# Optimization experiments

Measured on AMD Instinct MI355X. Metric: run time of the kernel, lower is better.

## Reference

```python
import jax, jax.numpy as jnp
import numpy as np

N, C, H, E = 10000, 128, 256, 320000
CUTOFF = 5.0
EPS = 1e-5


def _ln(x, g, b):
    mu = jnp.mean(x, axis=-1, keepdims=True)
    var = jnp.var(x, axis=-1, keepdims=True)
    return (x - mu) * jax.lax.rsqrt(var + EPS) * g + b


def setup_inputs() -> dict:
    key = jax.random.key(0)
    ks = jax.random.split(key, 24)

    def w(k, shape, fan_in):
        return (jax.random.normal(k, shape, dtype=jnp.float32) / np.sqrt(fan_in)).astype(jnp.float32)

    inp = {}
    inp["x"] = jax.random.normal(ks[0], (N, 3), dtype=jnp.float32)
    inp["h"] = jax.random.normal(ks[1], (N, C), dtype=jnp.float32)
    inp["edge_index"] = jax.random.randint(ks[2], (2, E), 0, N, dtype=jnp.int32)
    # edge_mlp: Linear(2C+1 -> H), SiLU, Linear(H -> H), SiLU
    inp["We1"] = w(ks[3], (2 * C + 1, H), 2 * C + 1); inp["be1"] = jnp.zeros((H,), jnp.float32)
    inp["We2"] = w(ks[4], (H, H), H);                inp["be2"] = jnp.zeros((H,), jnp.float32)
    # node_mlp: Linear(C+H -> H), SiLU, Linear(H -> C)
    inp["Wn1"] = w(ks[5], (C + H, H), C + H);        inp["bn1"] = jnp.zeros((H,), jnp.float32)
    inp["Wn2"] = w(ks[6], (H, C), H);                inp["bn2"] = jnp.zeros((C,), jnp.float32)
    # residual mlp: Linear(C -> H), SiLU, Dropout(eval), Linear(H -> C)
    inp["Wm1"] = w(ks[7], (C, H), C);                inp["bm1"] = jnp.zeros((H,), jnp.float32)
    inp["Wm2"] = w(ks[8], (H, C), H);                inp["bm2"] = jnp.zeros((C,), jnp.float32)
    # layernorms
    inp["g1"] = jnp.ones((C,), jnp.float32); inp["beta1"] = jnp.zeros((C,), jnp.float32)
    inp["g2"] = jnp.ones((C,), jnp.float32); inp["beta2"] = jnp.zeros((C,), jnp.float32)
    return inp


def reference(x, h, edge_index, We1, be1, We2, be2, Wn1, bn1, Wn2, bn2,
              Wm1, bm1, Wm2, bm2, g1, beta1, g2, beta2):
    row, col = edge_index[0], edge_index[1]

    h_res = h
    hn = _ln(h, g1, beta1)                              # [N, C]

    # ---- EGNN layer ----
    rel = x[row] - x[col]                               # [E, 3]
    dist = jnp.linalg.norm(rel, axis=-1, keepdims=True) # [E, 1]
    edge_in = jnp.concatenate([hn[row], hn[col], dist], axis=-1)  # [E, 2C+1]
    m = jax.nn.silu(edge_in @ We1 + be1)
    m = jax.nn.silu(m @ We2 + be2)                      # [E, H]

    d = dist[:, 0]
    Ccut = 0.5 * (jnp.cos(d * jnp.pi / CUTOFF) + 1.0)
    Ccut = Ccut * (d <= CUTOFF) * (d >= 0.0)
    m = m * Ccut[:, None]

    # mean-aggregate messages at target nodes (edge_index[1])
    sums = jax.ops.segment_sum(m, col, num_segments=N)          # [N, H]
    cnt = jax.ops.segment_sum(jnp.ones((m.shape[0],), m.dtype), col, num_segments=N)
    m_aggr = sums / jnp.maximum(cnt, 1.0)[:, None]

    hd = jax.nn.silu(jnp.concatenate([hn, m_aggr], axis=-1) @ Wn1 + bn1) @ Wn2 + bn2
    h_egnn = hn + hd

    h1 = h_res + h_egnn

    # ---- norm2 + MLP residual (dropout = identity in eval) ----
    h2 = _ln(h1, g2, beta2)
    h2 = jax.nn.silu(h2 @ Wm1 + bm1) @ Wm2 + bm2
    return h1 + h2
```

## Files before the change

### kernel.cpp

```cpp
#include <hip/hip_runtime.h>

#define NN 10000
#define CC 128
#define HH 256
#define EE 320000
#define ETILE 96
#define EBLOCKS 3334

typedef __bf16 bf16_t;
typedef __bf16 bf16x8 __attribute__((ext_vector_type(8)));
typedef __bf16 bf16x4 __attribute__((ext_vector_type(4)));
typedef float f32x4 __attribute__((ext_vector_type(4)));

__device__ __forceinline__ float silu_f(float v) {
#if __has_builtin(__builtin_amdgcn_rcpf)
  return v * __builtin_amdgcn_rcpf(1.0f + __expf(-v));
#else
  return v / (1.0f + __expf(-v));
#endif
}

template<int RE, int KD, int SA, int NT>
__device__ __forceinline__ void gemm_lg(const bf16_t* sAa, const bf16_t* __restrict__ BT,
                                        int nwavebase, int lr, int quad, f32x4 acc[RE][NT]) {
  for (int kk = 0; kk < KD; kk += 32) {
    bf16x8 a[RE]; bf16x8 b[NT];
#pragma unroll
    for (int re = 0; re < RE; re++)
      a[re] = *(const bf16x8*)(sAa + (re * 16 + lr) * SA + kk + quad * 8);
#pragma unroll
    for (int ce = 0; ce < NT; ce++)
      b[ce] = *(const bf16x8*)(BT + (size_t)(nwavebase + ce * 16 + lr) * KD + kk + quad * 8);
#pragma unroll
    for (int re = 0; re < RE; re++)
#pragma unroll
      for (int ce = 0; ce < NT; ce++)
        acc[re][ce] = __builtin_amdgcn_mfma_f32_16x16x32_bf16(a[re], b[ce], acc[re][ce], 0, 0, 0);
  }
}

__global__ __launch_bounds__(256) void prep_weights(
    const float* __restrict__ We1, const float* __restrict__ We2,
    const float* __restrict__ Wn1, const float* __restrict__ Wn2,
    const float* __restrict__ Wm1, const float* __restrict__ Wm2,
    bf16_t* __restrict__ We1T, bf16_t* __restrict__ We2T,
    bf16_t* __restrict__ Wn1T, bf16_t* __restrict__ Wn2T,
    bf16_t* __restrict__ Wm1T, bf16_t* __restrict__ Wm2T) {
  int i = blockIdx.x * 256 + threadIdx.x;
  const float* src; bf16_t* dst; int K, Nc, idx;
  if      (i < 65536)  { src = We1; dst = We1T; K = 256; Nc = 256; idx = i; }
  else if (i < 131072) { src = We2; dst = We2T; K = 256; Nc = 256; idx = i - 65536; }
  else if (i < 229376) { src = Wn1; dst = Wn1T; K = 384; Nc = 256; idx = i - 131072; }
  else if (i < 262144) { src = Wn2; dst = Wn2T; K = 256; Nc = 128; idx = i - 229376; }
  else if (i < 294912) { src = Wm1; dst = Wm1T; K = 128; Nc = 256; idx = i - 262144; }
  else                 { src = Wm2; dst = Wm2T; K = 256; Nc = 128; idx = i - 294912; }
  int n = idx / K, k = idx - n * K;
  dst[idx] = (bf16_t)src[(size_t)k * Nc + n];
}

__global__ __launch_bounds__(256, 3) void node_pre_kernel(
    const float* __restrict__ h, const float* __restrict__ g1,
    const float* __restrict__ bt1,
    const bf16_t* __restrict__ We1T, const float* __restrict__ be1,
    bf16_t* __restrict__ hn16, bf16_t* __restrict__ PQ) {
  __shared__ __align__(16) float sHf[64 * 132];
  __shared__ __align__(16) bf16_t sHn[64 * 136];
  int tid = threadIdx.x;
  int lane = tid & 63, wave = tid >> 6;
  int lr = lane & 15, quad = lane >> 4;
  int n0 = blockIdx.x * 64;

#pragma unroll
  for (int i = 0; i < 8; i++) {
    int o = tid + i * 256;
    int node = o >> 5, q = o & 31;
    f32x4 v = {0.f, 0.f, 0.f, 0.f};
    if (n0 + node < NN) v = *(const f32x4*)(h + (size_t)(n0 + node) * CC + q * 4);
    *(f32x4*)(sHf + node * 132 + q * 4) = v;
  }
  __syncthreads();

  {
    int node = tid >> 2, c0 = (tid & 3) * 32;
    f32x4 u[8];
    float s = 0.f, sq = 0.f;
#pragma unroll
    for (int j = 0; j < 8; j++) {
      u[j] = *(const f32x4*)(sHf + node * 132 + c0 + j * 4);
#pragma unroll
      for (int r = 0; r < 4; r++) { s += u[j][r]; sq += u[j][r] * u[j][r]; }
    }
    s += __shfl_xor(s, 1); sq += __shfl_xor(sq, 1);
    s += __shfl_xor(s, 2); sq += __shfl_xor(sq, 2);
    float mu = s * (1.0f / CC);
    float var = sq * (1.0f / CC) - mu * mu;
    float rs = rsqrtf(var + 1e-5f);
    bool live = (n0 + node) < NN;
#pragma unroll
    for (int j2 = 0; j2 < 4; j2++) {
      f32x4 gg0 = *(const f32x4*)(g1 + c0 + j2 * 8);
      f32x4 gg1 = *(const f32x4*)(g1 + c0 + j2 * 8 + 4);
      f32x4 bb0 = *(const f32x4*)(bt1 + c0 + j2 * 8);
      f32x4 bb1 = *(const f32x4*)(bt1 + c0 + j2 * 8 + 4);
      bf16x8 ov;
#pragma unroll
      for (int r = 0; r < 4; r++) {
        ov[r] = (bf16_t)((u[j2 * 2][r] - mu) * rs * gg0[r] + bb0[r]);
        ov[r + 4] = (bf16_t)((u[j2 * 2 + 1][r] - mu) * rs * gg1[r] + bb1[r]);
      }
      *(bf16x8*)(sHn + node * 136 + c0 + j2 * 8) = ov;
      if (live) *(bf16x8*)(hn16 + (size_t)(n0 + node) * CC + c0 + j2 * 8) = ov;
    }
  }
  __syncthreads();

  f32x4 zf = {0.f, 0.f, 0.f, 0.f};
#pragma unroll
  for (int p = 0; p < 2; p++) {
    f32x4 acc[4][4];
#pragma unroll
    for (int i = 0; i < 4; i++)
#pragma unroll
      for (int j = 0; j < 4; j++) acc[i][j] = zf;
    for (int kk = 0; kk < 128; kk += 32) {
      bf16x8 a[4]; bf16x8 b[4];
#pragma unroll
      for (int re = 0; re < 4; re++)
        a[re] = *(const bf16x8*)(We1T + (size_t)(wave * 64 + re * 16 + lr) * 256 + p * 128 + kk + quad * 8);
#pragma unroll
      for (int ce = 0; ce < 4; ce++)
        b[ce] = *(const bf16x8*)(sHn + (ce * 16 + lr) * 136 + kk + quad * 8);
#pragma unroll
      for (int re = 0; re < 4; re++)
#pragma unroll
        for (int ce = 0; ce < 4; ce++)
          acc[re][ce] = __builtin_amdgcn_mfma_f32_16x16x32_bf16(a[re], b[ce], acc[re][ce], 0, 0, 0);
    }
#pragma unroll
    for (int re = 0; re < 4; re++) {
      int cbase = wave * 64 + re * 16 + quad * 4;
      f32x4 bb = zf;
      if (p == 0) bb = *(const f32x4*)(be1 + cbase);
#pragma unroll
      for (int ce = 0; ce < 4; ce++) {
        int node = ce * 16 + lr;
        if (n0 + node < NN) {
          bf16x4 o;
#pragma unroll
          for (int r = 0; r < 4; r++) o[r] = (bf16_t)(acc[re][ce][r] + bb[r]);
          *(bf16x4*)(PQ + (size_t)(n0 + node) * 512 + p * 256 + cbase) = o;
        }
      }
    }
  }
}

__global__ __launch_bounds__(256) void count_kernel(const int* __restrict__ ei, int* __restrict__ cnt) {
  int e = blockIdx.x * 256 + threadIdx.x;
  atomicAdd(&cnt[ei[EE + e]], 1);
}

__global__ __launch_bounds__(1024) void scan_kernel(const int* __restrict__ cnt, int* __restrict__ cursor) {
  __shared__ int wsum[16];
  int tid = threadIdx.x, wave = tid >> 6, lane = tid & 63;
  int base = 0;
  for (int start = 0; start < NN; start += 1024) {
    int i = start + tid;
    int v = (i < NN) ? cnt[i] : 0;
    int s = v;
#pragma unroll
    for (int off = 1; off < 64; off <<= 1) { int t = __shfl_up(s, off); if (lane >= off) s += t; }
    if (lane == 63) wsum[wave] = s;
    __syncthreads();
    if (tid < 16) {
      int ws = wsum[tid];
#pragma unroll
      for (int off = 1; off < 16; off <<= 1) { int t = __shfl_up(ws, off); if (tid >= off) ws += t; }
      wsum[tid] = ws;
    }
    __syncthreads();
    int wp = (wave > 0) ? wsum[wave - 1] : 0;
    if (i < NN) cursor[i] = base + wp + s - v;
    base += wsum[15];
    __syncthreads();
  }
}

__global__ __launch_bounds__(256) void scatter_kernel(const int* __restrict__ ei,
                                                      const float* __restrict__ x,
                                                      int* __restrict__ cursor,
                                                      uint4* __restrict__ edat) {
  int e = blockIdx.x * 256 + threadIdx.x;
  int r = ei[e], c = ei[EE + e];
  float dx = x[3 * r] - x[3 * c];
  float dy = x[3 * r + 1] - x[3 * c + 1];
  float dz = x[3 * r + 2] - x[3 * c + 2];
  float d = sqrtf(dx * dx + dy * dy + dz * dz);
  float cc = (d <= 5.0f) ? 0.5f * (cosf(d * 0.6283185307179586f) + 1.0f) : 0.0f;
  int pos = atomicAdd(&cursor[c], 1);
  uint4 v = {(unsigned)r, (unsigned)c, __float_as_uint(d), __float_as_uint(cc)};
  edat[pos] = v;
}

__global__ __launch_bounds__(256, 3) void edge_mlp_kernel(
    const uint4* __restrict__ edat, const bf16_t* __restrict__ PQ,
    const float* __restrict__ We1last,
    const bf16_t* __restrict__ We2T, const float* __restrict__ be2,
    float* __restrict__ sums) {
  __shared__ __align__(16) bf16_t sM1[ETILE * 264];
  __shared__ int sRow[ETILE], sCol[ETILE];
  __shared__ float sD[ETILE], sCc[ETILE];
  __shared__ unsigned long long sMask[2];
  int tid = threadIdx.x;
  int lane = tid & 63, wave = tid >> 6;
  int lr = lane & 15, quad = lane >> 4;
  int e0 = blockIdx.x * ETILE;

  if (tid < ETILE) {
    uint4 v = edat[e0 + tid];
    sRow[tid] = (int)v.x; sCol[tid] = (int)v.y;
    sD[tid] = __uint_as_float(v.z); sCc[tid] = __uint_as_float(v.w);
  }
  __syncthreads();

  if (tid < ETILE) {
    int fl = (tid > 0) && (sCol[tid] != sCol[tid - 1]);
    unsigned long long m = __ballot(fl);
    if ((tid & 63) == 0) sMask[wave] = m;
  }

#pragma unroll
  for (int i = 0; i < ETILE * 32 / 256; i++) {
    int o = tid + i * 256;
    int e = o >> 5, q = o & 31;
    int k0 = q * 8;
    int row = sRow[e], col = sCol[e];
    float d = sD[e];
    bf16x8 pv = *(const bf16x8*)(PQ + (size_t)row * 512 + k0);
    bf16x8 qv = *(const bf16x8*)(PQ + (size_t)col * 512 + 256 + k0);
    f32x4 wl0 = *(const f32x4*)(We1last + k0);
    f32x4 wl1 = *(const f32x4*)(We1last + k0 + 4);
    bf16x8 m;
#pragma unroll
    for (int j = 0; j < 4; j++) {
      m[j] = (bf16_t)silu_f((float)pv[j] + (float)qv[j] + d * wl0[j]);
      m[j + 4] = (bf16_t)silu_f((float)pv[j + 4] + (float)qv[j + 4] + d * wl1[j]);
    }
    *(bf16x8*)(sM1 + e * 264 + k0) = m;
  }
  __syncthreads();

  f32x4 zf = {0.f, 0.f, 0.f, 0.f};
  f32x4 acc[6][4];
#pragma unroll
  for (int i = 0; i < 6; i++)
#pragma unroll
    for (int j = 0; j < 4; j++) acc[i][j] = zf;
  gemm_lg<6, 256, 264, 4>(sM1, We2T, wave * 64, lr, quad, acc);

  float be2v[4];
#pragma unroll
  for (int ce = 0; ce < 4; ce++) be2v[ce] = be2[wave * 64 + ce * 16 + lr];
#pragma unroll
  for (int re = 0; re < 6; re++) {
    f32x4 cc = *(const f32x4*)(sCc + re * 16 + quad * 4);
#pragma unroll
    for (int ce = 0; ce < 4; ce++)
#pragma unroll
      for (int r = 0; r < 4; r++)
        acc[re][ce][r] = silu_f(acc[re][ce][r] + be2v[ce]) * cc[r];
  }

  {
    unsigned long long w0 = sMask[0];
    unsigned long long w1 = sMask[1];
    int lo = 0;
    while (lo < ETILE) {
      int hi;
      unsigned long long t = (lo < 63) ? (w0 & (~0ull << (lo + 1))) : 0ull;
      if (t) {
        hi = __ffsll((long long)t) - 1;
      } else {
        unsigned long long mk = (lo + 1 > 64) ? (~0ull << (lo + 1 - 64)) : ~0ull;
        unsigned long long t1 = w1 & mk;
        hi = t1 ? 64 + __ffsll((long long)t1) - 1 : ETILE;
      }
      f32x4 tv = zf;
#pragma unroll
      for (int re = 0; re < 6; re++) {
        int eb = re * 16 + quad * 4;
#pragma unroll
        for (int r = 0; r < 4; r++) {
          int e = eb + r;
          bool in = (e >= lo) && (e < hi);
#pragma unroll
          for (int ce = 0; ce < 4; ce++)
            tv[ce] += in ? acc[re][ce][r] : 0.0f;
        }
      }
#pragma unroll
      for (int ce = 0; ce < 4; ce++) {
        tv[ce] += __shfl_xor(tv[ce], 16);
        tv[ce] += __shfl_xor(tv[ce], 32);
      }
      if (quad == 0) {
        int colv = sCol[lo];
#pragma unroll
        for (int ce = 0; ce < 4; ce++)
          atomicAdd(&sums[(size_t)colv * HH + wave * 64 + ce * 16 + lr], tv[ce]);
      }
      lo = hi;
    }
  }
}

__global__ __launch_bounds__(256) void node_fused_kernel(
    const float* __restrict__ h, const bf16_t* __restrict__ hn16,
    const float* __restrict__ sums, const int* __restrict__ cnt,
    const bf16_t* __restrict__ Wn1T, const float* __restrict__ bn1,
    const bf16_t* __restrict__ Wn2T, const float* __restrict__ bn2,
    const float* __restrict__ g2, const float* __restrict__ bt2,
    const bf16_t* __restrict__ Wm1T, const float* __restrict__ bm1,
    const bf16_t* __restrict__ Wm2T, const float* __restrict__ bm2,
    float* __restrict__ out) {
  __shared__ __align__(16) bf16_t sA1[16 * 392];
  __shared__ __align__(16) bf16_t sM[16 * 264];
  __shared__ __align__(16) float sH1[16 * 132];
  __shared__ __align__(16) bf16_t sLn[16 * 136];
  __shared__ float sRc[16];
  int tid = threadIdx.x;
  int lane = tid & 63, wave = tid >> 6;
  int lr = lane & 15, quad = lane >> 4;
  int n0 = blockIdx.x * 16;

  if (tid < 16) sRc[tid] = 1.0f / fmaxf((float)cnt[n0 + tid], 1.0f);
  __syncthreads();

#pragma unroll
  for (int i = 0; i < 3; i++) {
    int o = tid + i * 256;
    int e = o / 48, q = o - e * 48;
    int node = n0 + e;
    if (q < 16) {
      *(uint4*)(sA1 + e * 392 + q * 8) = *(const uint4*)(hn16 + (size_t)node * CC + q * 8);
    } else {
      float rc = sRc[e];
      const float* sp = sums + (size_t)node * HH + (q - 16) * 8;
      bf16x8 bv;
#pragma unroll
      for (int k2 = 0; k2 < 8; k2++) bv[k2] = (bf16_t)(sp[k2] * rc);
      *(bf16x8*)(sA1 + e * 392 + (q - 16) * 8 + 128) = bv;
    }
  }
  __syncthreads();

  f32x4 zf = {0.f, 0.f, 0.f, 0.f};
  {
    f32x4 acc[1][4];
#pragma unroll
    for (int j = 0; j < 4; j++) acc[0][j] = zf;
    gemm_lg<1, 384, 392, 4>(sA1, Wn1T, wave * 64, lr, quad, acc);
#pragma unroll
    for (int ce = 0; ce < 4; ce++) {
      int n = wave * 64 + ce * 16 + lr;
      float b1 = bn1[n];
#pragma unroll
      for (int r = 0; r < 4; r++)
        sM[(quad * 4 + r) * 264 + n] = (bf16_t)silu_f(acc[0][ce][r] + b1);
    }
  }
  __syncthreads();

  {
    f32x4 acc[1][2];
    acc[0][0] = zf; acc[0][1] = zf;
    gemm_lg<1, 256, 264, 2>(sM, Wn2T, wave * 32, lr, quad, acc);
#pragma unroll
    for (int ce = 0; ce < 2; ce++) {
      int n = wave * 32 + ce * 16 + lr;
      float b2 = bn2[n];
#pragma unroll
      for (int r = 0; r < 4; r++) {
        int node = quad * 4 + r;
        size_t idx = (size_t)(n0 + node) * CC + n;
        float hn_v = (float)sA1[node * 392 + n];
        sH1[node * 132 + n] = h[idx] + hn_v + acc[0][ce][r] + b2;
      }
    }
  }
  __syncthreads();

  {
    int node = tid >> 4, c0 = (tid & 15) * 8;
    f32x4 u0 = *(const f32x4*)(sH1 + node * 132 + c0);
    f32x4 u1 = *(const f32x4*)(sH1 + node * 132 + c0 + 4);
    float s = 0.f, sq = 0.f;
#pragma unroll
    for (int j = 0; j < 4; j++) { s += u0[j] + u1[j]; sq += u0[j] * u0[j] + u1[j] * u1[j]; }
#pragma unroll
    for (int o = 8; o > 0; o >>= 1) { s += __shfl_xor(s, o); sq += __shfl_xor(sq, o); }
    float mu = s * (1.0f / CC);
    float var = sq * (1.0f / CC) - mu * mu;
    float rs = rsqrtf(var + 1e-5f);
    f32x4 gg0 = *(const f32x4*)(g2 + c0), gg1 = *(const f32x4*)(g2 + c0 + 4);
    f32x4 bb0 = *(const f32x4*)(bt2 + c0), bb1 = *(const f32x4*)(bt2 + c0 + 4);
    bf16x8 ov;
#pragma unroll
    for (int j = 0; j < 4; j++) {
      ov[j] = (bf16_t)((u0[j] - mu) * rs * gg0[j] + bb0[j]);
      ov[j + 4] = (bf16_t)((u1[j] - mu) * rs * gg1[j] + bb1[j]);
    }
    *(bf16x8*)(sLn + node * 136 + c0) = ov;
  }
  __syncthreads();

  {
    f32x4 acc[1][4];
#pragma unroll
    for (int j = 0; j < 4; j++) acc[0][j] = zf;
    gemm_lg<1, 128, 136, 4>(sLn, Wm1T, wave * 64, lr, quad, acc);
#pragma unroll
    for (int ce = 0; ce < 4; ce++) {
      int n = wave * 64 + ce * 16 + lr;
      float b1 = bm1[n];
#pragma unroll
      for (int r = 0; r < 4; r++)
        sM[(quad * 4 + r) * 264 + n] = (bf16_t)silu_f(acc[0][ce][r] + b1);
    }
  }
  __syncthreads();

  {
    f32x4 acc[1][2];
    acc[0][0] = zf; acc[0][1] = zf;
    gemm_lg<1, 256, 264, 2>(sM, Wm2T, wave * 32, lr, quad, acc);
#pragma unroll
    for (int ce = 0; ce < 2; ce++) {
      int n = wave * 32 + ce * 16 + lr;
      float b2 = bm2[n];
#pragma unroll
      for (int r = 0; r < 4; r++) {
        int node = quad * 4 + r;
        size_t idx = (size_t)(n0 + node) * CC + n;
        out[idx] = sH1[node * 132 + n] + acc[0][ce][r] + b2;
      }
    }
  }
}

extern "C" void kernel_launch(void* const* d_in, const int* in_sizes, int n_in,
                              void* d_out, int out_size, void* d_ws, size_t ws_size,
                              hipStream_t stream) {
  const float* x    = (const float*)d_in[0];
  const float* h    = (const float*)d_in[1];
  const int*   ei   = (const int*)d_in[2];
  const float* We1  = (const float*)d_in[3];
  const float* be1  = (const float*)d_in[4];
  const float* We2  = (const float*)d_in[5];
  const float* be2  = (const float*)d_in[6];
  const float* Wn1  = (const float*)d_in[7];
  const float* bn1  = (const float*)d_in[8];
  const float* Wn2  = (const float*)d_in[9];
  const float* bn2  = (const float*)d_in[10];
  const float* Wm1  = (const float*)d_in[11];
  const float* bm1  = (const float*)d_in[12];
  const float* Wm2  = (const float*)d_in[13];
  const float* bm2  = (const float*)d_in[14];
  const float* g1   = (const float*)d_in[15];
  const float* bt1  = (const float*)d_in[16];
  const float* g2   = (const float*)d_in[17];
  const float* bt2  = (const float*)d_in[18];
  float* out = (float*)d_out;

  char* wp = (char*)d_ws;
  size_t off = 0;
  auto alloc = [&](size_t bytes) -> void* {
    void* p = wp + off;
    off = (off + bytes + 255) & ~(size_t)255;
    return p;
  };

  bf16_t* hn16   = (bf16_t*)alloc((size_t)NN * CC * 2);
  bf16_t* PQ     = (bf16_t*)alloc((size_t)NN * 512 * 2);
  float*  sums   = (float*)alloc((size_t)NN * HH * 4);
  int*    cnt    = (int*)alloc((size_t)NN * 4);
  int*    cursor = (int*)alloc((size_t)NN * 4);
  uint4*  edat   = (uint4*)alloc((size_t)(EBLOCKS * ETILE) * 16);
  bf16_t* We1T   = (bf16_t*)alloc(256 * 256 * 2);
  bf16_t* We2T   = (bf16_t*)alloc(256 * 256 * 2);
  bf16_t* Wn1T   = (bf16_t*)alloc(256 * 384 * 2);
  bf16_t* Wn2T   = (bf16_t*)alloc(128 * 256 * 2);
  bf16_t* Wm1T   = (bf16_t*)alloc(256 * 128 * 2);
  bf16_t* Wm2T   = (bf16_t*)alloc(128 * 256 * 2);

  hipMemsetAsync(sums, 0, (size_t)NN * HH * 4, stream);
  hipMemsetAsync(cnt, 0, (size_t)NN * 4, stream);
  hipMemsetAsync(edat + EE, 0, (size_t)(EBLOCKS * ETILE - EE) * 16, stream);

  prep_weights<<<1280, 256, 0, stream>>>(We1, We2, Wn1, Wn2, Wm1, Wm2,
                                         We1T, We2T, Wn1T, Wn2T, Wm1T, Wm2T);

  node_pre_kernel<<<(NN + 63) / 64, 256, 0, stream>>>(h, g1, bt1, We1T, be1, hn16, PQ);

  count_kernel<<<EE / 256, 256, 0, stream>>>(ei, cnt);
  scan_kernel<<<1, 1024, 0, stream>>>(cnt, cursor);
  scatter_kernel<<<EE / 256, 256, 0, stream>>>(ei, x, cursor, edat);

  edge_mlp_kernel<<<EBLOCKS, 256, 0, stream>>>(edat, PQ, We1 + 256 * 256,
                                               We2T, be2, sums);

  node_fused_kernel<<<NN / 16, 256, 0, stream>>>(h, hn16, sums, cnt,
                                                 Wn1T, bn1, Wn2T, bn2,
                                                 g2, bt2, Wm1T, bm1, Wm2T, bm2, out);
}
```

Before: 311.7 us.

## Retile edge and node kernels, fold memsets into weight prep kernel

Shrinks the edge MLP tile from 96 to 64 edges (one mask word, 4 blocks per CU occupancy hint) and grows the node fused kernel from 16 to 64 nodes per block so each weight load feeds four MFMA row tiles. It also replaces the separate memset calls with zeroing inside the weight-prep kernel, cutting launch count. The larger node tile uses about 135KB of shared memory, which limits it to one block per CU, and the smaller edge tile means more segments cut at tile edges and more atomics.

```diff
diff --git a/kernel.cpp b/kernel.cpp
--- a/kernel.cpp
+++ b/kernel.cpp
@@ -4,8 +4,8 @@
 #define CC 128
 #define HH 256
 #define EE 320000
-#define ETILE 96
-#define EBLOCKS 3334
+#define ETILE 64
+#define EBLOCKS 5000
 
 typedef __bf16 bf16_t;
 typedef __bf16 bf16x8 __attribute__((ext_vector_type(8)));
@@ -39,23 +39,32 @@
   }
 }
 
-__global__ __launch_bounds__(256) void prep_weights(
+__global__ __launch_bounds__(256) void prep_kernel(
     const float* __restrict__ We1, const float* __restrict__ We2,
     const float* __restrict__ Wn1, const float* __restrict__ Wn2,
     const float* __restrict__ Wm1, const float* __restrict__ Wm2,
     bf16_t* __restrict__ We1T, bf16_t* __restrict__ We2T,
     bf16_t* __restrict__ Wn1T, bf16_t* __restrict__ Wn2T,
-    bf16_t* __restrict__ Wm1T, bf16_t* __restrict__ Wm2T) {
+    bf16_t* __restrict__ Wm1T, bf16_t* __restrict__ Wm2T,
+    float* __restrict__ sums, int* __restrict__ cnt) {
   int i = blockIdx.x * 256 + threadIdx.x;
-  const float* src; bf16_t* dst; int K, Nc, idx;
-  if      (i < 65536)  { src = We1; dst = We1T; K = 256; Nc = 256; idx = i; }
-  else if (i < 131072) { src = We2; dst = We2T; K = 256; Nc = 256; idx = i - 65536; }
-  else if (i < 229376) { src = Wn1; dst = Wn1T; K = 384; Nc = 256; idx = i - 131072; }
-  else if (i < 262144) { src = Wn2; dst = Wn2T; K = 256; Nc = 128; idx = i - 229376; }
-  else if (i < 294912) { src = Wm1; dst = Wm1T; K = 128; Nc = 256; idx = i - 262144; }
-  else                 { src = Wm2; dst = Wm2T; K = 256; Nc = 128; idx = i - 294912; }
-  int n = idx / K, k = idx - n * K;
-  dst[idx] = (bf16_t)src[(size_t)k * Nc + n];
+  if (i < 327680) {
+    const float* src; bf16_t* dst; int K, Nc, idx;
+    if      (i < 65536)  { src = We1; dst = We1T; K = 256; Nc = 256; idx = i; }
+    else if (i < 131072) { src = We2; dst = We2T; K = 256; Nc = 256; idx = i - 65536; }
+    else if (i < 229376) { src = Wn1; dst = Wn1T; K = 384; Nc = 256; idx = i - 131072; }
+    else if (i < 262144) { src = Wn2; dst = Wn2T; K = 256; Nc = 128; idx = i - 229376; }
+    else if (i < 294912) { src = Wm1; dst = Wm1T; K = 128; Nc = 256; idx = i - 262144; }
+    else                 { src = Wm2; dst = Wm2T; K = 256; Nc = 128; idx = i - 294912; }
+    int n = idx / K, k = idx - n * K;
+    dst[idx] = (bf16_t)src[(size_t)k * Nc + n];
+  } else if (i < 327680 + 640000) {
+    f32x4 z = {0.f, 0.f, 0.f, 0.f};
+    ((f32x4*)sums)[i - 327680] = z;
+  } else if (i < 327680 + 640000 + 2500) {
+    int4 z = {0, 0, 0, 0};
+    ((int4*)cnt)[i - 967680] = z;
+  }
 }
 
 __global__ __launch_bounds__(256, 3) void node_pre_kernel(
@@ -202,7 +211,7 @@
   edat[pos] = v;
 }
 
-__global__ __launch_bounds__(256, 3) void edge_mlp_kernel(
+__global__ __launch_bounds__(256, 4) void edge_mlp_kernel(
     const uint4* __restrict__ edat, const bf16_t* __restrict__ PQ,
     const float* __restrict__ We1last,
     const bf16_t* __restrict__ We2T, const float* __restrict__ be2,
@@ -210,7 +219,7 @@
   __shared__ __align__(16) bf16_t sM1[ETILE * 264];
   __shared__ int sRow[ETILE], sCol[ETILE];
   __shared__ float sD[ETILE], sCc[ETILE];
-  __shared__ unsigned long long sMask[2];
+  __shared__ unsigned long long sMask;
   int tid = threadIdx.x;
   int lane = tid & 63, wave = tid >> 6;
   int lr = lane & 15, quad = lane >> 4;
@@ -223,14 +232,14 @@
   }
   __syncthreads();
 
-  if (tid < ETILE) {
+  if (tid < 64) {
     int fl = (tid > 0) && (sCol[tid] != sCol[tid - 1]);
     unsigned long long m = __ballot(fl);
-    if ((tid & 63) == 0) sMask[wave] = m;
-  }
-
-#pragma unroll
-  for (int i = 0; i < ETILE * 32 / 256; i++) {
+    if (tid == 0) sMask = m;
+  }
+
+#pragma unroll
+  for (int i = 0; i < 8; i++) {
     int o = tid + i * 256;
     int e = o >> 5, q = o & 31;
     int k0 = q * 8;
@@ -251,18 +260,18 @@
   __syncthreads();
 
   f32x4 zf = {0.f, 0.f, 0.f, 0.f};
-  f32x4 acc[6][4];
-#pragma unroll
-  for (int i = 0; i < 6; i++)
+  f32x4 acc[4][4];
+#pragma unroll
+  for (int i = 0; i < 4; i++)
 #pragma unroll
     for (int j = 0; j < 4; j++) acc[i][j] = zf;
-  gemm_lg<6, 256, 264, 4>(sM1, We2T, wave * 64, lr, quad, acc);
+  gemm_lg<4, 256, 264, 4>(sM1, We2T, wave * 64, lr, quad, acc);
 
   float be2v[4];
 #pragma unroll
   for (int ce = 0; ce < 4; ce++) be2v[ce] = be2[wave * 64 + ce * 16 + lr];
 #pragma unroll
-  for (int re = 0; re < 6; re++) {
+  for (int re = 0; re < 4; re++) {
     f32x4 cc = *(const f32x4*)(sCc + re * 16 + quad * 4);
 #pragma unroll
     for (int ce = 0; ce < 4; ce++)
@@ -272,22 +281,14 @@
   }
 
   {
-    unsigned long long w0 = sMask[0];
-    unsigned long long w1 = sMask[1];
+    unsigned long long w0 = sMask;
     int lo = 0;
     while (lo < ETILE) {
-      int hi;
       unsigned long long t = (lo < 63) ? (w0 & (~0ull << (lo + 1))) : 0ull;
-      if (t) {
-        hi = __ffsll((long long)t) - 1;
-      } else {
-        unsigned long long mk = (lo + 1 > 64) ? (~0ull << (lo + 1 - 64)) : ~0ull;
-        unsigned long long t1 = w1 & mk;
-        hi = t1 ? 64 + __ffsll((long long)t1) - 1 : ETILE;
-      }
+      int hi = t ? (__ffsll((long long)t) - 1) : ETILE;
       f32x4 tv = zf;
 #pragma unroll
-      for (int re = 0; re < 6; re++) {
+      for (int re = 0; re < 4; re++) {
         int eb = re * 16 + quad * 4;
 #pragma unroll
         for (int r = 0; r < 4; r++) {
@@ -314,7 +315,7 @@
   }
 }
 
-__global__ __launch_bounds__(256) void node_fused_kernel(
+__global__ __launch_bounds__(256, 1) void node_fused_kernel(
     const float* __restrict__ h, const bf16_t* __restrict__ hn16,
     const float* __restrict__ sums, const int* __restrict__ cnt,
     const bf16_t* __restrict__ Wn1T, const float* __restrict__ bn1,
@@ -323,127 +324,171 @@
     const bf16_t* __restrict__ Wm1T, const float* __restrict__ bm1,
     const bf16_t* __restrict__ Wm2T, const float* __restrict__ bm2,
     float* __restrict__ out) {
-  __shared__ __align__(16) bf16_t sA1[16 * 392];
-  __shared__ __align__(16) bf16_t sM[16 * 264];
-  __shared__ __align__(16) float sH1[16 * 132];
-  __shared__ __align__(16) bf16_t sLn[16 * 136];
-  __shared__ float sRc[16];
+  __shared__ __align__(16) char smem[135168];
+  bf16_t* sA1 = (bf16_t*)smem;
+  bf16_t* sM1b = (bf16_t*)(smem + 50176);
+  float*  sH1 = (float*)(smem + 50176);
+  bf16_t* sLn = (bf16_t*)(smem + 83968);
+  bf16_t* sH2 = (bf16_t*)(smem + 101376);
+  __shared__ float sRc[64];
   int tid = threadIdx.x;
   int lane = tid & 63, wave = tid >> 6;
   int lr = lane & 15, quad = lane >> 4;
-  int n0 = blockIdx.x * 16;
-
-  if (tid < 16) sRc[tid] = 1.0f / fmaxf((float)cnt[n0 + tid], 1.0f);
-  __syncthreads();
-
-#pragma unroll
-  for (int i = 0; i < 3; i++) {
+  int n0 = blockIdx.x * 64;
+
+  if (tid < 64) {
+    int node = n0 + tid;
+    sRc[tid] = (node < NN) ? 1.0f / fmaxf((float)cnt[node], 1.0f) : 0.0f;
+  }
+  __syncthreads();
+
+#pragma unroll
+  for (int i = 0; i < 12; i++) {
     int o = tid + i * 256;
     int e = o / 48, q = o - e * 48;
     int node = n0 + e;
     if (q < 16) {
-      *(uint4*)(sA1 + e * 392 + q * 8) = *(const uint4*)(hn16 + (size_t)node * CC + q * 8);
+      uint4 v = {0u, 0u, 0u, 0u};
+      if (node < NN) v = *(const uint4*)(hn16 + (size_t)node * CC + q * 8);
+      *(uint4*)(sA1 + e * 392 + q * 8) = v;
     } else {
-      float rc = sRc[e];
-      const float* sp = sums + (size_t)node * HH + (q - 16) * 8;
-      bf16x8 bv;
-#pragma unroll
-      for (int k2 = 0; k2 < 8; k2++) bv[k2] = (bf16_t)(sp[k2] * rc);
-      *(bf16x8*)(sA1 + e * 392 + (q - 16) * 8 + 128) = bv;
+      bf16x8 bv = {};
+      if (node < NN) {
+        float rc = sRc[e];
+        const float* sp = sums + (size_t)node * HH + (q - 16) * 8;
+#pragma unroll
+        for (int k2 = 0; k2 < 8; k2++) bv[k2] = (bf16_t)(sp[k2] * rc);
+      }
+      *(bf16x8*)(sA1 + e * 392 + 128 + (q - 16) * 8) = bv;
     }
   }
   __syncthreads();
 
   f32x4 zf = {0.f, 0.f, 0.f, 0.f};
   {
-    f32x4 acc[1][4];
-#pragma unroll
-    for (int j = 0; j < 4; j++) acc[0][j] = zf;
-    gemm_lg<1, 384, 392, 4>(sA1, Wn1T, wave * 64, lr, quad, acc);
+    f32x4 acc[4][4];
+#pragma unroll
+    for (int i = 0; i < 4; i++)
+#pragma unroll
+      for (int j = 0; j < 4; j++) acc[i][j] = zf;
+    gemm_lg<4, 384, 392, 4>(sA1, Wn1T, wave * 64, lr, quad, acc);
+    __syncthreads();
 #pragma unroll
     for (int ce = 0; ce < 4; ce++) {
       int n = wave * 64 + ce * 16 + lr;
       float b1 = bn1[n];
 #pragma unroll
-      for (int r = 0; r < 4; r++)
-        sM[(quad * 4 + r) * 264 + n] = (bf16_t)silu_f(acc[0][ce][r] + b1);
-    }
-  }
-  __syncthreads();
-
-  {
-    f32x4 acc[1][2];
-    acc[0][0] = zf; acc[0][1] = zf;
-    gemm_lg<1, 256, 264, 2>(sM, Wn2T, wave * 32, lr, quad, acc);
+      for (int re = 0; re < 4; re++)
+#pragma unroll
+        for (int r = 0; r < 4; r++)
+          sM1b[(re * 16 + quad * 4 + r) * 264 + n] = (bf16_t)silu_f(acc[re][ce][r] + b1);
+    }
+  }
+  __syncthreads();
+
+  float h1v[4][2][4];
+  {
+    f32x4 acc[4][2];
+#pragma unroll
+    for (int i = 0; i < 4; i++) { acc[i][0] = zf; acc[i][1] = zf; }
+    gemm_lg<4, 256, 264, 2>(sM1b, Wn2T, wave * 32, lr, quad, acc);
 #pragma unroll
     for (int ce = 0; ce < 2; ce++) {
       int n = wave * 32 + ce * 16 + lr;
       float b2 = bn2[n];
 #pragma unroll
-      for (int r = 0; r < 4; r++) {
-        int node = quad * 4 + r;
-        size_t idx = (size_t)(n0 + node) * CC + n;
-        float hn_v = (float)sA1[node * 392 + n];
-        sH1[node * 132 + n] = h[idx] + hn_v + acc[0][ce][r] + b2;
-      }
-    }
-  }
-  __syncthreads();
-
-  {
-    int node = tid >> 4, c0 = (tid & 15) * 8;
-    f32x4 u0 = *(const f32x4*)(sH1 + node * 132 + c0);
-    f32x4 u1 = *(const f32x4*)(sH1 + node * 132 + c0 + 4);
+      for (int re = 0; re < 4; re++)
+#pragma unroll
+        for (int r = 0; r < 4; r++) {
+          int node = re * 16 + quad * 4 + r;
+          float hv = 0.f;
+          if (n0 + node < NN) hv = h[(size_t)(n0 + node) * CC + n];
+          h1v[re][ce][r] = hv + (float)sA1[node * 392 + n] + acc[re][ce][r] + b2;
+        }
+    }
+  }
+  __syncthreads();
+
+#pragma unroll
+  for (int ce = 0; ce < 2; ce++) {
+    int n = wave * 32 + ce * 16 + lr;
+#pragma unroll
+    for (int re = 0; re < 4; re++)
+#pragma unroll
+      for (int r = 0; r < 4; r++)
+        sH1[(re * 16 + quad * 4 + r) * 132 + n] = h1v[re][ce][r];
+  }
+  __syncthreads();
+
+  {
+    int node = tid >> 2, c0 = (tid & 3) * 32;
+    f32x4 u[8];
     float s = 0.f, sq = 0.f;
 #pragma unroll
-    for (int j = 0; j < 4; j++) { s += u0[j] + u1[j]; sq += u0[j] * u0[j] + u1[j] * u1[j]; }
-#pragma unroll
-    for (int o = 8; o > 0; o >>= 1) { s += __shfl_xor(s, o); sq += __shfl_xor(sq, o); }
+    for (int j = 0; j < 8; j++) {
+      u[j] = *(const f32x4*)(sH1 + node * 132 + c0 + j * 4);
+#pragma unroll
+      for (int r = 0; r < 4; r++) { s += u[j][r]; sq += u[j][r] * u[j][r]; }
+    }
+    s += __shfl_xor(s, 1); sq += __shfl_xor(sq, 1);
+    s += __shfl_xor(s, 2); sq += __shfl_xor(sq, 2);
     float mu = s * (1.0f / CC);
     float var = sq * (1.0f / CC) - mu * mu;
     float rs = rsqrtf(var + 1e-5f);
-    f32x4 gg0 = *(const f32x4*)(g2 + c0), gg1 = *(const f32x4*)(g2 + c0 + 4);
-    f32x4 bb0 = *(const f32x4*)(bt2 + c0), bb1 = *(const f32x4*)(bt2 + c0 + 4);
-    bf16x8 ov;
-#pragma unroll
-    for (int j = 0; j < 4; j++) {
-      ov[j] = (bf16_t)((u0[j] - mu) * rs * gg0[j] + bb0[j]);
-      ov[j + 4] = (bf16_t)((u1[j] - mu) * rs * gg1[j] + bb1[j]);
-    }
-    *(bf16x8*)(sLn + node * 136 + c0) = ov;
-  }
-  __syncthreads();
-
-  {
-    f32x4 acc[1][4];
-#pragma unroll
-    for (int j = 0; j < 4; j++) acc[0][j] = zf;
-    gemm_lg<1, 128, 136, 4>(sLn, Wm1T, wave * 64, lr, quad, acc);
+#pragma unroll
+    for (int j2 = 0; j2 < 4; j2++) {
+      f32x4 gg0 = *(const f32x4*)(g2 + c0 + j2 * 8);
+      f32x4 gg1 = *(const f32x4*)(g2 + c0 + j2 * 8 + 4);
+      f32x4 bb0 = *(const f32x4*)(bt2 + c0 + j2 * 8);
+      f32x4 bb1 = *(const f32x4*)(bt2 + c0 + j2 * 8 + 4);
+      bf16x8 ov;
+#pragma unroll
+      for (int r = 0; r < 4; r++) {
+        ov[r] = (bf16_t)((u[j2 * 2][r] - mu) * rs * gg0[r] + bb0[r]);
+        ov[r + 4] = (bf16_t)((u[j2 * 2 + 1][r] - mu) * rs * gg1[r] + bb1[r]);
+      }
+      *(bf16x8*)(sLn + node * 136 + c0 + j2 * 8) = ov;
+    }
+  }
+  __syncthreads();
+
+  {
+    f32x4 acc[4][4];
+#pragma unroll
+    for (int i = 0; i < 4; i++)
+#pragma unroll
+      for (int j = 0; j < 4; j++) acc[i][j] = zf;
+    gemm_lg<4, 128, 136, 4>(sLn, Wm1T, wave * 64, lr, quad, acc);
 #pragma unroll
     for (int ce = 0; ce < 4; ce++) {
       int n = wave * 64 + ce * 16 + lr;
       float b1 = bm1[n];
 #pragma unroll
-      for (int r = 0; r < 4; r++)
-        sM[(quad * 4 + r) * 264 + n] = (bf16_t)silu_f(acc[0][ce][r] + b1);
-    }
-  }
-  __syncthreads();
-
-  {
-    f32x4 acc[1][2];
-    acc[0][0] = zf; acc[0][1] = zf;
-    gemm_lg<1, 256, 264, 2>(sM, Wm2T, wave * 32, lr, quad, acc);
+      for (int re = 0; re < 4; re++)
+#pragma unroll
+        for (int r = 0; r < 4; r++)
+          sH2[(re * 16 + quad * 4 + r) * 264 + n] = (bf16_t)silu_f(acc[re][ce][r] + b1);
+    }
+  }
+  __syncthreads();
+
+  {
+    f32x4 acc[4][2];
+#pragma unroll
+    for (int i = 0; i < 4; i++) { acc[i][0] = zf; acc[i][1] = zf; }
+    gemm_lg<4, 256, 264, 2>(sH2, Wm2T, wave * 32, lr, quad, acc);
 #pragma unroll
     for (int ce = 0; ce < 2; ce++) {
       int n = wave * 32 + ce * 16 + lr;
       float b2 = bm2[n];
 #pragma unroll
-      for (int r = 0; r < 4; r++) {
-        int node = quad * 4 + r;
-        size_t idx = (size_t)(n0 + node) * CC + n;
-        out[idx] = sH1[node * 132 + n] + acc[0][ce][r] + b2;
-      }
+      for (int re = 0; re < 4; re++)
+#pragma unroll
+        for (int r = 0; r < 4; r++) {
+          int node = re * 16 + quad * 4 + r;
+          if (n0 + node < NN)
+            out[(size_t)(n0 + node) * CC + n] = sH1[node * 132 + n] + acc[re][ce][r] + b2;
+        }
     }
   }
 }
@@ -485,7 +530,7 @@
   float*  sums   = (float*)alloc((size_t)NN * HH * 4);
   int*    cnt    = (int*)alloc((size_t)NN * 4);
   int*    cursor = (int*)alloc((size_t)NN * 4);
-  uint4*  edat   = (uint4*)alloc((size_t)(EBLOCKS * ETILE) * 16);
+  uint4*  edat   = (uint4*)alloc((size_t)EE * 16);
   bf16_t* We1T   = (bf16_t*)alloc(256 * 256 * 2);
   bf16_t* We2T   = (bf16_t*)alloc(256 * 256 * 2);
   bf16_t* Wn1T   = (bf16_t*)alloc(256 * 384 * 2);
@@ -493,12 +538,9 @@
   bf16_t* Wm1T   = (bf16_t*)alloc(256 * 128 * 2);
   bf16_t* Wm2T   = (bf16_t*)alloc(128 * 256 * 2);
 
-  hipMemsetAsync(sums, 0, (size_t)NN * HH * 4, stream);
-  hipMemsetAsync(cnt, 0, (size_t)NN * 4, stream);
-  hipMemsetAsync(edat + EE, 0, (size_t)(EBLOCKS * ETILE - EE) * 16, stream);
-
-  prep_weights<<<1280, 256, 0, stream>>>(We1, We2, Wn1, Wn2, Wm1, Wm2,
-                                         We1T, We2T, Wn1T, Wn2T, Wm1T, Wm2T);
+  prep_kernel<<<3790, 256, 0, stream>>>(We1, We2, Wn1, Wn2, Wm1, Wm2,
+                                        We1T, We2T, Wn1T, Wn2T, Wm1T, Wm2T,
+                                        sums, cnt);
 
   node_pre_kernel<<<(NN + 63) / 64, 256, 0, stream>>>(h, g1, bt1, We1T, be1, hn16, PQ);
 
@@ -509,7 +551,7 @@
   edge_mlp_kernel<<<EBLOCKS, 256, 0, stream>>>(edat, PQ, We1 + 256 * 256,
                                                We2T, be2, sums);
 
-  node_fused_kernel<<<NN / 16, 256, 0, stream>>>(h, hn16, sums, cnt,
-                                                 Wn1T, bn1, Wn2T, bn2,
-                                                 g2, bt2, Wm1T, bm1, Wm2T, bm2, out);
-}
+  node_fused_kernel<<<(NN + 63) / 64, 256, 0, stream>>>(h, hn16, sums, cnt,
+                                                        Wn1T, bn1, Wn2T, bn2,
+                                                        g2, bt2, Wm1T, bm1, Wm2T, bm2, out);
+}
```

After: 311.0 us. About the same (-0.2%).

## Fold memsets into prep kernel, retile node_pre, single-pass scan, faster segment reduce

Applied to the files above, without the earlier changes.

Replaces three hipMemsetAsync calls with zeroing work folded into the weight-prep kernel, which removes separate launches. The node_pre kernel is retiled to 16 nodes per block with direct global loads and a per-wave split of P/Q outputs. The scan becomes a single pass with 10 elements per thread, and the edge segment reduction skips or fully sums 16-row tiles instead of masking every element. Occupancy hints are also adjusted. Together these trade larger per-thread work and more blocks for fewer launches and less masking overhead.

```diff
diff --git a/kernel.cpp b/kernel.cpp
--- a/kernel.cpp
+++ b/kernel.cpp
@@ -39,119 +39,99 @@
   }
 }
 
-__global__ __launch_bounds__(256) void prep_weights(
+__global__ __launch_bounds__(256) void prep_kernel(
     const float* __restrict__ We1, const float* __restrict__ We2,
     const float* __restrict__ Wn1, const float* __restrict__ Wn2,
     const float* __restrict__ Wm1, const float* __restrict__ Wm2,
     bf16_t* __restrict__ We1T, bf16_t* __restrict__ We2T,
     bf16_t* __restrict__ Wn1T, bf16_t* __restrict__ Wn2T,
-    bf16_t* __restrict__ Wm1T, bf16_t* __restrict__ Wm2T) {
+    bf16_t* __restrict__ Wm1T, bf16_t* __restrict__ Wm2T,
+    float* __restrict__ sums, int* __restrict__ cnt, uint4* __restrict__ edat) {
   int i = blockIdx.x * 256 + threadIdx.x;
-  const float* src; bf16_t* dst; int K, Nc, idx;
-  if      (i < 65536)  { src = We1; dst = We1T; K = 256; Nc = 256; idx = i; }
-  else if (i < 131072) { src = We2; dst = We2T; K = 256; Nc = 256; idx = i - 65536; }
-  else if (i < 229376) { src = Wn1; dst = Wn1T; K = 384; Nc = 256; idx = i - 131072; }
-  else if (i < 262144) { src = Wn2; dst = Wn2T; K = 256; Nc = 128; idx = i - 229376; }
-  else if (i < 294912) { src = Wm1; dst = Wm1T; K = 128; Nc = 256; idx = i - 262144; }
-  else                 { src = Wm2; dst = Wm2T; K = 256; Nc = 128; idx = i - 294912; }
-  int n = idx / K, k = idx - n * K;
-  dst[idx] = (bf16_t)src[(size_t)k * Nc + n];
-}
-
-__global__ __launch_bounds__(256, 3) void node_pre_kernel(
+  if (i < 327680) {
+    const float* src; bf16_t* dst; int K, Nc, idx;
+    if      (i < 65536)  { src = We1; dst = We1T; K = 256; Nc = 256; idx = i; }
+    else if (i < 131072) { src = We2; dst = We2T; K = 256; Nc = 256; idx = i - 65536; }
+    else if (i < 229376) { src = Wn1; dst = Wn1T; K = 384; Nc = 256; idx = i - 131072; }
+    else if (i < 262144) { src = Wn2; dst = Wn2T; K = 256; Nc = 128; idx = i - 229376; }
+    else if (i < 294912) { src = Wm1; dst = Wm1T; K = 128; Nc = 256; idx = i - 262144; }
+    else                 { src = Wm2; dst = Wm2T; K = 256; Nc = 128; idx = i - 294912; }
+    int n = idx / K, k = idx - n * K;
+    dst[idx] = (bf16_t)src[(size_t)k * Nc + n];
+  } else if (i < 327680 + 640000) {
+    f32x4 z = {0.f, 0.f, 0.f, 0.f};
+    ((f32x4*)sums)[i - 327680] = z;
+  } else if (i < 327680 + 640000 + 2500) {
+    int4 z = {0, 0, 0, 0};
+    ((int4*)cnt)[i - 967680] = z;
+  } else if (i < 327680 + 640000 + 2500 + 64) {
+    uint4 z = {0u, 0u, 0u, 0u};
+    edat[EE + (i - 970180)] = z;
+  }
+}
+
+__global__ __launch_bounds__(256, 4) void node_pre_kernel(
     const float* __restrict__ h, const float* __restrict__ g1,
     const float* __restrict__ bt1,
     const bf16_t* __restrict__ We1T, const float* __restrict__ be1,
     bf16_t* __restrict__ hn16, bf16_t* __restrict__ PQ) {
-  __shared__ __align__(16) float sHf[64 * 132];
-  __shared__ __align__(16) bf16_t sHn[64 * 136];
+  __shared__ __align__(16) bf16_t sHn[16 * 136];
   int tid = threadIdx.x;
   int lane = tid & 63, wave = tid >> 6;
   int lr = lane & 15, quad = lane >> 4;
-  int n0 = blockIdx.x * 64;
-
-#pragma unroll
-  for (int i = 0; i < 8; i++) {
-    int o = tid + i * 256;
-    int node = o >> 5, q = o & 31;
-    f32x4 v = {0.f, 0.f, 0.f, 0.f};
-    if (n0 + node < NN) v = *(const f32x4*)(h + (size_t)(n0 + node) * CC + q * 4);
-    *(f32x4*)(sHf + node * 132 + q * 4) = v;
-  }
-  __syncthreads();
-
-  {
-    int node = tid >> 2, c0 = (tid & 3) * 32;
-    f32x4 u[8];
+  int n0 = blockIdx.x * 16;
+
+  {
+    int node = tid >> 4, c0 = (tid & 15) * 8;
+    size_t base = (size_t)(n0 + node) * CC;
+    f32x4 u0 = *(const f32x4*)(h + base + c0);
+    f32x4 u1 = *(const f32x4*)(h + base + c0 + 4);
     float s = 0.f, sq = 0.f;
 #pragma unroll
-    for (int j = 0; j < 8; j++) {
-      u[j] = *(const f32x4*)(sHf + node * 132 + c0 + j * 4);
-#pragma unroll
-      for (int r = 0; r < 4; r++) { s += u[j][r]; sq += u[j][r] * u[j][r]; }
-    }
-    s += __shfl_xor(s, 1); sq += __shfl_xor(sq, 1);
-    s += __shfl_xor(s, 2); sq += __shfl_xor(sq, 2);
+    for (int j = 0; j < 4; j++) { s += u0[j] + u1[j]; sq += u0[j] * u0[j] + u1[j] * u1[j]; }
+#pragma unroll
+    for (int o = 8; o > 0; o >>= 1) { s += __shfl_xor(s, o); sq += __shfl_xor(sq, o); }
     float mu = s * (1.0f / CC);
     float var = sq * (1.0f / CC) - mu * mu;
     float rs = rsqrtf(var + 1e-5f);
-    bool live = (n0 + node) < NN;
-#pragma unroll
-    for (int j2 = 0; j2 < 4; j2++) {
-      f32x4 gg0 = *(const f32x4*)(g1 + c0 + j2 * 8);
-      f32x4 gg1 = *(const f32x4*)(g1 + c0 + j2 * 8 + 4);
-      f32x4 bb0 = *(const f32x4*)(bt1 + c0 + j2 * 8);
-      f32x4 bb1 = *(const f32x4*)(bt1 + c0 + j2 * 8 + 4);
-      bf16x8 ov;
-#pragma unroll
-      for (int r = 0; r < 4; r++) {
-        ov[r] = (bf16_t)((u[j2 * 2][r] - mu) * rs * gg0[r] + bb0[r]);
-        ov[r + 4] = (bf16_t)((u[j2 * 2 + 1][r] - mu) * rs * gg1[r] + bb1[r]);
-      }
-      *(bf16x8*)(sHn + node * 136 + c0 + j2 * 8) = ov;
-      if (live) *(bf16x8*)(hn16 + (size_t)(n0 + node) * CC + c0 + j2 * 8) = ov;
-    }
-  }
-  __syncthreads();
-
+    f32x4 gg0 = *(const f32x4*)(g1 + c0), gg1 = *(const f32x4*)(g1 + c0 + 4);
+    f32x4 bb0 = *(const f32x4*)(bt1 + c0), bb1 = *(const f32x4*)(bt1 + c0 + 4);
+    bf16x8 ov;
+#pragma unroll
+    for (int j = 0; j < 4; j++) {
+      ov[j] = (bf16_t)((u0[j] - mu) * rs * gg0[j] + bb0[j]);
+      ov[j + 4] = (bf16_t)((u1[j] - mu) * rs * gg1[j] + bb1[j]);
+    }
+    *(bf16x8*)(sHn + node * 136 + c0) = ov;
+    *(bf16x8*)(hn16 + base + c0) = ov;
+  }
+  __syncthreads();
+
+  bool isQ = wave >= 2;
+  int rbase = (wave & 1) * 128;
+  int koff = isQ ? 128 : 0;
   f32x4 zf = {0.f, 0.f, 0.f, 0.f};
-#pragma unroll
-  for (int p = 0; p < 2; p++) {
-    f32x4 acc[4][4];
-#pragma unroll
-    for (int i = 0; i < 4; i++)
-#pragma unroll
-      for (int j = 0; j < 4; j++) acc[i][j] = zf;
-    for (int kk = 0; kk < 128; kk += 32) {
-      bf16x8 a[4]; bf16x8 b[4];
-#pragma unroll
-      for (int re = 0; re < 4; re++)
-        a[re] = *(const bf16x8*)(We1T + (size_t)(wave * 64 + re * 16 + lr) * 256 + p * 128 + kk + quad * 8);
-#pragma unroll
-      for (int ce = 0; ce < 4; ce++)
-        b[ce] = *(const bf16x8*)(sHn + (ce * 16 + lr) * 136 + kk + quad * 8);
-#pragma unroll
-      for (int re = 0; re < 4; re++)
-#pragma unroll
-        for (int ce = 0; ce < 4; ce++)
-          acc[re][ce] = __builtin_amdgcn_mfma_f32_16x16x32_bf16(a[re], b[ce], acc[re][ce], 0, 0, 0);
-    }
-#pragma unroll
-    for (int re = 0; re < 4; re++) {
-      int cbase = wave * 64 + re * 16 + quad * 4;
-      f32x4 bb = zf;
-      if (p == 0) bb = *(const f32x4*)(be1 + cbase);
-#pragma unroll
-      for (int ce = 0; ce < 4; ce++) {
-        int node = ce * 16 + lr;
-        if (n0 + node < NN) {
-          bf16x4 o;
-#pragma unroll
-          for (int r = 0; r < 4; r++) o[r] = (bf16_t)(acc[re][ce][r] + bb[r]);
-          *(bf16x4*)(PQ + (size_t)(n0 + node) * 512 + p * 256 + cbase) = o;
-        }
-      }
-    }
+  f32x4 acc[8];
+#pragma unroll
+  for (int i = 0; i < 8; i++) acc[i] = zf;
+  for (int kk = 0; kk < 128; kk += 32) {
+    bf16x8 b = *(const bf16x8*)(sHn + lr * 136 + kk + quad * 8);
+    bf16x8 a[8];
+#pragma unroll
+    for (int re = 0; re < 8; re++)
+      a[re] = *(const bf16x8*)(We1T + (size_t)(rbase + re * 16 + lr) * 256 + koff + kk + quad * 8);
+#pragma unroll
+    for (int re = 0; re < 8; re++)
+      acc[re] = __builtin_amdgcn_mfma_f32_16x16x32_bf16(a[re], b, acc[re], 0, 0, 0);
+  }
+#pragma unroll
+  for (int re = 0; re < 8; re++) {
+    int cb = rbase + re * 16 + quad * 4;
+    f32x4 bb = isQ ? zf : *(const f32x4*)(be1 + cb);
+    bf16x4 o;
+#pragma unroll
+    for (int r = 0; r < 4; r++) o[r] = (bf16_t)(acc[re][r] + bb[r]);
+    *(bf16x4*)(PQ + (size_t)(n0 + lr) * 512 + (isQ ? 256 : 0) + cb) = o;
   }
 }
 
@@ -163,26 +143,32 @@
 __global__ __launch_bounds__(1024) void scan_kernel(const int* __restrict__ cnt, int* __restrict__ cursor) {
   __shared__ int wsum[16];
   int tid = threadIdx.x, wave = tid >> 6, lane = tid & 63;
-  int base = 0;
-  for (int start = 0; start < NN; start += 1024) {
-    int i = start + tid;
-    int v = (i < NN) ? cnt[i] : 0;
-    int s = v;
-#pragma unroll
-    for (int off = 1; off < 64; off <<= 1) { int t = __shfl_up(s, off); if (lane >= off) s += t; }
-    if (lane == 63) wsum[wave] = s;
-    __syncthreads();
-    if (tid < 16) {
-      int ws = wsum[tid];
-#pragma unroll
-      for (int off = 1; off < 16; off <<= 1) { int t = __shfl_up(ws, off); if (tid >= off) ws += t; }
-      wsum[tid] = ws;
-    }
-    __syncthreads();
-    int wp = (wave > 0) ? wsum[wave - 1] : 0;
-    if (i < NN) cursor[i] = base + wp + s - v;
-    base += wsum[15];
-    __syncthreads();
+  int base = tid * 10;
+  int v[10]; int S = 0;
+#pragma unroll
+  for (int j = 0; j < 10; j++) {
+    int i = base + j;
+    v[j] = (i < NN) ? cnt[i] : 0;
+    S += v[j];
+  }
+  int s = S;
+#pragma unroll
+  for (int off = 1; off < 64; off <<= 1) { int t = __shfl_up(s, off); if (lane >= off) s += t; }
+  if (lane == 63) wsum[wave] = s;
+  __syncthreads();
+  if (tid < 16) {
+    int ws = wsum[tid];
+#pragma unroll
+    for (int off = 1; off < 16; off <<= 1) { int t = __shfl_up(ws, off); if (tid >= off) ws += t; }
+    wsum[tid] = ws;
+  }
+  __syncthreads();
+  int ex = ((wave > 0) ? wsum[wave - 1] : 0) + s - S;
+#pragma unroll
+  for (int j = 0; j < 10; j++) {
+    int i = base + j;
+    if (i < NN) cursor[i] = ex;
+    ex += v[j];
   }
 }
 
@@ -210,7 +196,8 @@
   __shared__ __align__(16) bf16_t sM1[ETILE * 264];
   __shared__ int sRow[ETILE], sCol[ETILE];
   __shared__ float sD[ETILE], sCc[ETILE];
-  __shared__ unsigned long long sMask[2];
+  __shared__ unsigned long long sMaskA;
+  __shared__ unsigned sMaskB;
   int tid = threadIdx.x;
   int lane = tid & 63, wave = tid >> 6;
   int lr = lane & 15, quad = lane >> 4;
@@ -226,7 +213,8 @@
   if (tid < ETILE) {
     int fl = (tid > 0) && (sCol[tid] != sCol[tid - 1]);
     unsigned long long m = __ballot(fl);
-    if ((tid & 63) == 0) sMask[wave] = m;
+    if (tid == 0) sMaskA = m;
+    if (tid == 64) sMaskB = (unsigned)m;
   }
 
 #pragma unroll
@@ -272,30 +260,40 @@
   }
 
   {
-    unsigned long long w0 = sMask[0];
-    unsigned long long w1 = sMask[1];
+    unsigned long long mA = sMaskA;
+    unsigned long long mB = (unsigned long long)sMaskB;
     int lo = 0;
     while (lo < ETILE) {
       int hi;
-      unsigned long long t = (lo < 63) ? (w0 & (~0ull << (lo + 1))) : 0ull;
-      if (t) {
-        hi = __ffsll((long long)t) - 1;
+      if (lo < 63) {
+        unsigned long long t = mA & (~0ull << (lo + 1));
+        hi = t ? (__ffsll((long long)t) - 1)
+               : (mB ? 64 + __ffsll((long long)mB) - 1 : ETILE);
       } else {
-        unsigned long long mk = (lo + 1 > 64) ? (~0ull << (lo + 1 - 64)) : ~0ull;
-        unsigned long long t1 = w1 & mk;
+        unsigned long long t1 = mB & (~0ull << (lo - 63));
         hi = t1 ? 64 + __ffsll((long long)t1) - 1 : ETILE;
       }
       f32x4 tv = zf;
 #pragma unroll
       for (int re = 0; re < 6; re++) {
-        int eb = re * 16 + quad * 4;
-#pragma unroll
-        for (int r = 0; r < 4; r++) {
-          int e = eb + r;
-          bool in = (e >= lo) && (e < hi);
-#pragma unroll
-          for (int ce = 0; ce < 4; ce++)
-            tv[ce] += in ? acc[re][ce][r] : 0.0f;
+        int t0 = re * 16, t1e = t0 + 16;
+        if (t1e <= lo || t0 >= hi) continue;
+        if (t0 >= lo && t1e <= hi) {
+#pragma unroll
+          for (int r = 0; r < 4; r++)
+#pragma unroll
+            for (int ce = 0; ce < 4; ce++)
+              tv[ce] += acc[re][ce][r];
+        } else {
+          int eb = t0 + quad * 4;
+#pragma unroll
+          for (int r = 0; r < 4; r++) {
+            int e = eb + r;
+            bool in = (e >= lo) && (e < hi);
+#pragma unroll
+            for (int ce = 0; ce < 4; ce++)
+              tv[ce] += in ? acc[re][ce][r] : 0.0f;
+          }
         }
       }
 #pragma unroll
@@ -314,7 +312,7 @@
   }
 }
 
-__global__ __launch_bounds__(256) void node_fused_kernel(
+__global__ __launch_bounds__(256, 3) void node_fused_kernel(
     const float* __restrict__ h, const bf16_t* __restrict__ hn16,
     const float* __restrict__ sums, const int* __restrict__ cnt,
     const bf16_t* __restrict__ Wn1T, const float* __restrict__ bn1,
@@ -349,7 +347,7 @@
       bf16x8 bv;
 #pragma unroll
       for (int k2 = 0; k2 < 8; k2++) bv[k2] = (bf16_t)(sp[k2] * rc);
-      *(bf16x8*)(sA1 + e * 392 + (q - 16) * 8 + 128) = bv;
+      *(bf16x8*)(sA1 + e * 392 + 128 + (q - 16) * 8) = bv;
     }
   }
   __syncthreads();
@@ -493,14 +491,11 @@
   bf16_t* Wm1T   = (bf16_t*)alloc(256 * 128 * 2);
   bf16_t* Wm2T   = (bf16_t*)alloc(128 * 256 * 2);
 
-  hipMemsetAsync(sums, 0, (size_t)NN * HH * 4, stream);
-  hipMemsetAsync(cnt, 0, (size_t)NN * 4, stream);
-  hipMemsetAsync(edat + EE, 0, (size_t)(EBLOCKS * ETILE - EE) * 16, stream);
-
-  prep_weights<<<1280, 256, 0, stream>>>(We1, We2, Wn1, Wn2, Wm1, Wm2,
-                                         We1T, We2T, Wn1T, Wn2T, Wm1T, Wm2T);
-
-  node_pre_kernel<<<(NN + 63) / 64, 256, 0, stream>>>(h, g1, bt1, We1T, be1, hn16, PQ);
+  prep_kernel<<<3791, 256, 0, stream>>>(We1, We2, Wn1, Wn2, Wm1, Wm2,
+                                        We1T, We2T, Wn1T, Wn2T, Wm1T, Wm2T,
+                                        sums, cnt, edat);
+
+  node_pre_kernel<<<NN / 16, 256, 0, stream>>>(h, g1, bt1, We1T, be1, hn16, PQ);
 
   count_kernel<<<EE / 256, 256, 0, stream>>>(ei, cnt);
   scan_kernel<<<1, 1024, 0, stream>>>(cnt, cursor);
```

After: 294.9 us. -5.4%, faster.
